# Optimization experiments

Hardware: AMD Instinct MI355X
Metric: run time of the kernel (lower is better)

## Reference

```python
import jax, jax.numpy as jnp
import numpy as np

EMB = 1024
HEADS = 16
HEADSIZE = EMB // HEADS
LN_EPS = 1e-5


def layernorm(x, w, b):
    # normalize over last dim (headsize)
    mu = jnp.mean(x, axis=-1, keepdims=True)
    var = jnp.var(x, axis=-1, keepdims=True)
    return (x - mu) * jax.lax.rsqrt(var + LN_EPS) * w + b


def setup_inputs() -> dict:
    key = jax.random.key(0)
    ks = jax.random.split(key, 8)
    B, S, C = 2, 2048, 2048
    x = jax.random.normal(ks[0], (B, S, EMB), dtype=jnp.float32)
    context = jax.random.normal(ks[1], (B, C, EMB), dtype=jnp.float32)
    mask = jnp.ones((B, S), dtype=jnp.float32)
    contextMask = jnp.ones((B, C), dtype=jnp.float32)
    s = 0.02
    Wq = jax.random.normal(ks[2], (EMB, EMB), dtype=jnp.float32) * s
    Wk = jax.random.normal(ks[3], (EMB, EMB), dtype=jnp.float32) * s
    Wv = jax.random.normal(ks[4], (EMB, EMB), dtype=jnp.float32) * s
    Wu = jax.random.normal(ks[5], (EMB, EMB), dtype=jnp.float32) * s
    bu = jnp.zeros((EMB,), dtype=jnp.float32)
    qln_w = jnp.ones((HEADSIZE,), dtype=jnp.float32)
    qln_b = jnp.zeros((HEADSIZE,), dtype=jnp.float32)
    kln_w = jnp.ones((HEADSIZE,), dtype=jnp.float32)
    kln_b = jnp.zeros((HEADSIZE,), dtype=jnp.float32)
    return {"x": x, "context": context, "mask": mask, "contextMask": contextMask,
            "Wq": Wq, "Wk": Wk, "Wv": Wv, "Wu": Wu, "bu": bu,
            "qln_w": qln_w, "qln_b": qln_b, "kln_w": kln_w, "kln_b": kln_b}


def reference(x, context, mask, contextMask, Wq, Wk, Wv, Wu, bu, qln_w, qln_b, kln_w, kln_b):
    B, S, E = x.shape
    C = context.shape[1]
    T = S + C
    xc = jnp.concatenate([x, context], axis=1)            # [B, T, E]
    q = (x @ Wq).reshape(B, S, HEADS, HEADSIZE)
    k = (xc @ Wk).reshape(B, T, HEADS, HEADSIZE)
    v = (xc @ Wv).reshape(B, T, HEADS, HEADSIZE)
    q = layernorm(q, qln_w, qln_b)
    k = layernorm(k, kln_w, kln_b)
    scale = E ** 0.25
    q = q / scale
    k = k / scale
    # [B, H, S, T] score matrix (explicitly materialized, as in the original)
    dot = jnp.einsum('bshd,bthd->bhst', q, k)
    mcat = jnp.concatenate([mask, contextMask], axis=1)   # [B, T]
    dotMask = mask[:, None, :, None] * mcat[:, None, None, :]  # [B,1,S,T]
    # hand-rolled masked softmax: softmax(dot*mask) * mask, renormalize
    p = jax.nn.softmax(dot * dotMask, axis=-1) * dotMask
    p = p / (jnp.sum(p, axis=-1, keepdims=True) + 1e-13)
    out = jnp.einsum('bhst,bthd->bshd', p, v).reshape(B, S, E)
    return out @ Wu + bu
```

## Files before the change

kernel.cpp:

```cpp
#include <hip/hip_runtime.h>
#include <hip/hip_bf16.h>
#include <cstdint>

#define B_SZ   2
#define S_LEN  2048
#define C_LEN  2048
#define T_LEN  4096
#define EMB_   1024
#define HEADS_ 16
#define D_     64

typedef __attribute__((ext_vector_type(8))) short bf16x8;
typedef __attribute__((ext_vector_type(4))) float f32x4;
typedef __attribute__((ext_vector_type(16))) float f32x16;
typedef __attribute__((ext_vector_type(2))) float f32x2;

__device__ __forceinline__ unsigned short f2bf(float f) {
    unsigned u = __builtin_bit_cast(unsigned, f);
    u += 0x7fffu + ((u >> 16) & 1u);
    return (unsigned short)(u >> 16);
}
__device__ __forceinline__ float bf2f(unsigned short h) {
    return __builtin_bit_cast(float, (unsigned)h << 16);
}

__global__ void build_xcb_k(const float* __restrict__ x, const float* __restrict__ ctx,
                            unsigned short* __restrict__ xcb) {
    int i = blockIdx.x * blockDim.x + threadIdx.x;
    size_t e8 = (size_t)i * 8;
    int b = (int)(e8 / ((size_t)T_LEN * EMB_));
    size_t rem = e8 % ((size_t)T_LEN * EMB_);
    int t = (int)(rem / EMB_);
    int c = (int)(rem % EMB_);
    const float* src = (t < S_LEN)
        ? &x[((size_t)b * S_LEN + t) * EMB_ + c]
        : &ctx[((size_t)b * C_LEN + (t - S_LEN)) * EMB_ + c];
    float4 v0 = ((const float4*)src)[0];
    float4 v1 = ((const float4*)src)[1];
    uint4 o;
    o.x = (unsigned)f2bf(v0.x) | ((unsigned)f2bf(v0.y) << 16);
    o.y = (unsigned)f2bf(v0.z) | ((unsigned)f2bf(v0.w) << 16);
    o.z = (unsigned)f2bf(v1.x) | ((unsigned)f2bf(v1.y) << 16);
    o.w = (unsigned)f2bf(v1.z) | ((unsigned)f2bf(v1.w) << 16);
    *(uint4*)&xcb[e8] = o;
}

__global__ void mcat_k(const float* __restrict__ mask, const float* __restrict__ cmask,
                       float* __restrict__ Mcat) {
    int i = blockIdx.x * 256 + threadIdx.x;
    int b = i / T_LEN, t = i % T_LEN;
    Mcat[i] = (t < S_LEN) ? mask[(size_t)b * S_LEN + t]
                          : cmask[(size_t)b * C_LEN + (t - S_LEN)];
}

__global__ void wtrans4_k(const float* __restrict__ W0, const float* __restrict__ W1,
                          const float* __restrict__ W2, const float* __restrict__ W3,
                          unsigned short* __restrict__ T0, unsigned short* __restrict__ T1,
                          unsigned short* __restrict__ T2, unsigned short* __restrict__ T3) {
    __shared__ __align__(16) unsigned short tile[64][72];
    int bx = blockIdx.x, by = blockIdx.y, bz = blockIdx.z;
    const float* W = (bz == 0) ? W0 : (bz == 1) ? W1 : (bz == 2) ? W2 : W3;
    unsigned short* WT = (bz == 0) ? T0 : (bz == 1) ? T1 : (bz == 2) ? T2 : T3;
    int tid = threadIdx.x;
#pragma unroll
    for (int r = 0; r < 4; ++r) {
        int idx = tid + r * 256;
        int row = idx >> 4, c4 = idx & 15;
        float4 v = ((const float4*)&W[((size_t)(by * 64 + row)) * EMB_ + bx * 64])[c4];
        tile[row][c4 * 4 + 0] = f2bf(v.x);
        tile[row][c4 * 4 + 1] = f2bf(v.y);
        tile[row][c4 * 4 + 2] = f2bf(v.z);
        tile[row][c4 * 4 + 3] = f2bf(v.w);
    }
    __syncthreads();
#pragma unroll
    for (int r = 0; r < 2; ++r) {
        int idx = tid + r * 256;
        int n = idx >> 3, k8 = idx & 7;
        uint4 o;
        unsigned q[4];
#pragma unroll
        for (int j = 0; j < 4; ++j)
            q[j] = (unsigned)tile[k8 * 8 + 2 * j][n] | ((unsigned)tile[k8 * 8 + 2 * j + 1][n] << 16);
        o.x = q[0]; o.y = q[1]; o.z = q[2]; o.w = q[3];
        *(uint4*)&WT[((size_t)(bx * 64 + n)) * EMB_ + by * 64 + k8 * 8] = o;
    }
}

__global__ __launch_bounds__(256) void gemm_qkv_k(
    const unsigned short* __restrict__ A,
    const unsigned short* __restrict__ Bt,
    unsigned short* __restrict__ Yk,
    unsigned short* __restrict__ Yv,
    unsigned short* __restrict__ Yq) {
    constexpr int KTOT = 1024, NTOT = 1024;
    int nt = blockIdx.x, mt = blockIdx.y;
    if (nt >= 16 && (mt & 31) >= 16) return;
    __shared__ __align__(16) unsigned short As[128 * 32];
    __shared__ __align__(16) unsigned short Bs[128 * 32];
    int in_row0 = mt * 128;
    unsigned short* Cout;
    int col0, out_row0;
    if (nt < 8)       { Cout = Yk; col0 = nt * 128;        out_row0 = mt * 128; }
    else if (nt < 16) { Cout = Yv; col0 = (nt - 8) * 128;  out_row0 = mt * 128; }
    else              { Cout = Yq; col0 = (nt - 16) * 128;
                        out_row0 = (mt >> 5) * 2048 + (mt & 31) * 128; }
    int tid = threadIdx.x, w = tid >> 6, l = tid & 63, l15 = l & 15, lg = l >> 4;
    int wr = (w >> 1) * 64, wc = (w & 1) * 64;

    f32x4 zero4 = {0.f, 0.f, 0.f, 0.f};
    f32x4 acc[4][4];
#pragma unroll
    for (int i = 0; i < 4; ++i)
#pragma unroll
        for (int j = 0; j < 4; ++j) acc[i][j] = zero4;

    for (int k0 = 0; k0 < KTOT; k0 += 32) {
#pragma unroll
        for (int j = 0; j < 2; ++j) {
            int o = tid * 16 + j * 4096;
            int row = o >> 6;
            int ke = (o & 63) >> 1;
            __builtin_amdgcn_global_load_lds(
                (const __attribute__((address_space(1))) void*)&A[(size_t)(in_row0 + row) * KTOT + k0 + ke],
                (__attribute__((address_space(3))) void*)&As[o >> 1], 16, 0, 0);
            __builtin_amdgcn_global_load_lds(
                (const __attribute__((address_space(1))) void*)&Bt[(size_t)(nt * 128 + row) * KTOT + k0 + ke],
                (__attribute__((address_space(3))) void*)&Bs[o >> 1], 16, 0, 0);
        }
        __syncthreads();
        bf16x8 af[4], bf[4];
#pragma unroll
        for (int fr = 0; fr < 4; ++fr)
            af[fr] = *(const bf16x8*)&As[(wr + fr * 16 + l15) * 32 + lg * 8];
#pragma unroll
        for (int fc = 0; fc < 4; ++fc)
            bf[fc] = *(const bf16x8*)&Bs[(wc + fc * 16 + l15) * 32 + lg * 8];
#pragma unroll
        for (int fr = 0; fr < 4; ++fr)
#pragma unroll
            for (int fc = 0; fc < 4; ++fc)
                acc[fr][fc] = __builtin_amdgcn_mfma_f32_16x16x32_bf16(af[fr], bf[fc], acc[fr][fc], 0, 0, 0);
        __syncthreads();
    }
#pragma unroll
    for (int fr = 0; fr < 4; ++fr) {
#pragma unroll
        for (int fc = 0; fc < 4; ++fc) {
            int row = out_row0 + wr + fr * 16 + lg * 4;
            int col = col0 + wc + fc * 16 + l15;
#pragma unroll
            for (int i = 0; i < 4; ++i)
                Cout[(size_t)(row + i) * NTOT + col] = f2bf(acc[fr][fc][i]);
        }
    }
}

template <bool F32OUT>
__global__ __launch_bounds__(256) void gemm_bt_k(
    const unsigned short* __restrict__ A,
    const unsigned short* __restrict__ Bt,
    void* __restrict__ Cout,
    const float* __restrict__ bias,
    int mtiles_per_chunk, int chunk_stride) {
    constexpr int KTOT = 1024, NTOT = 1024;
    __shared__ __align__(16) unsigned short As[128 * 32];
    __shared__ __align__(16) unsigned short Bs[128 * 32];
    int nt = blockIdx.x, mt = blockIdx.y;
    int in_row0 = (mt / mtiles_per_chunk) * chunk_stride + (mt % mtiles_per_chunk) * 128;
    int out_row0 = mt * 128;
    int tid = threadIdx.x, w = tid >> 6, l = tid & 63, l15 = l & 15, lg = l >> 4;
    int wr = (w >> 1) * 64, wc = (w & 1) * 64;

    f32x4 zero4 = {0.f, 0.f, 0.f, 0.f};
    f32x4 acc[4][4];
#pragma unroll
    for (int i = 0; i < 4; ++i)
#pragma unroll
        for (int j = 0; j < 4; ++j) acc[i][j] = zero4;

    for (int k0 = 0; k0 < KTOT; k0 += 32) {
#pragma unroll
        for (int j = 0; j < 2; ++j) {
            int o = tid * 16 + j * 4096;
            int row = o >> 6;
            int ke = (o & 63) >> 1;
            __builtin_amdgcn_global_load_lds(
                (const __attribute__((address_space(1))) void*)&A[(size_t)(in_row0 + row) * KTOT + k0 + ke],
                (__attribute__((address_space(3))) void*)&As[o >> 1], 16, 0, 0);
            __builtin_amdgcn_global_load_lds(
                (const __attribute__((address_space(1))) void*)&Bt[(size_t)(nt * 128 + row) * KTOT + k0 + ke],
                (__attribute__((address_space(3))) void*)&Bs[o >> 1], 16, 0, 0);
        }
        __syncthreads();
        bf16x8 af[4], bf[4];
#pragma unroll
        for (int fr = 0; fr < 4; ++fr)
            af[fr] = *(const bf16x8*)&As[(wr + fr * 16 + l15) * 32 + lg * 8];
#pragma unroll
        for (int fc = 0; fc < 4; ++fc)
            bf[fc] = *(const bf16x8*)&Bs[(wc + fc * 16 + l15) * 32 + lg * 8];
#pragma unroll
        for (int fr = 0; fr < 4; ++fr)
#pragma unroll
            for (int fc = 0; fc < 4; ++fc)
                acc[fr][fc] = __builtin_amdgcn_mfma_f32_16x16x32_bf16(af[fr], bf[fc], acc[fr][fc], 0, 0, 0);
        __syncthreads();
    }
#pragma unroll
    for (int fr = 0; fr < 4; ++fr) {
#pragma unroll
        for (int fc = 0; fc < 4; ++fc) {
            int row = out_row0 + wr + fr * 16 + lg * 4;
            int col = nt * 128 + wc + fc * 16 + l15;
#pragma unroll
            for (int i = 0; i < 4; ++i) {
                float v = acc[fr][fc][i];
                if (F32OUT) {
                    ((float*)Cout)[(size_t)(row + i) * NTOT + col] = v + bias[col];
                } else {
                    ((unsigned short*)Cout)[(size_t)(row + i) * NTOT + col] = f2bf(v);
                }
            }
        }
    }
}

__global__ void ln_head_k(const unsigned short* __restrict__ Y,
                          unsigned short* __restrict__ Out,
                          const float* __restrict__ lw, const float* __restrict__ lb,
                          const float* __restrict__ Mcat,
                          int rows_per_b, float scale) {
    int gw = blockIdx.x * 4 + (threadIdx.x >> 6);
    int lane = threadIdx.x & 63;
    int h = gw % HEADS_;
    int row = gw / HEADS_;
    int b = row / rows_per_b, r = row % rows_per_b;
    float v = bf2f(Y[(size_t)row * EMB_ + h * 64 + lane]);
    float s = v, s2 = v * v;
#pragma unroll
    for (int m = 1; m <= 32; m <<= 1) {
        s += __shfl_xor(s, m);
        s2 += __shfl_xor(s2, m);
    }
    float mu = s * (1.f / 64.f);
    float var = s2 * (1.f / 64.f) - mu * mu;
    float o = (v - mu) * rsqrtf(var + 1e-5f) * lw[lane] + lb[lane];
    float mq = Mcat[(size_t)b * T_LEN + r];
    Out[(((size_t)b * HEADS_ + h) * rows_per_b + r) * 64 + lane] = f2bf(o * scale * mq);
}

__global__ void ln_head_pack_k(const unsigned short* __restrict__ Y,
                               unsigned short* __restrict__ KF,
                               const float* __restrict__ lw, const float* __restrict__ lb,
                               const float* __restrict__ Mcat,
                               float scale) {
    int gw = blockIdx.x * 4 + (threadIdx.x >> 6);
    int lane = threadIdx.x & 63;
    int h = gw % HEADS_;
    int row = gw / HEADS_;
    int b = row / T_LEN, r = row % T_LEN;
    float v = bf2f(Y[(size_t)row * EMB_ + h * 64 + lane]);
    float s = v, s2 = v * v;
#pragma unroll
    for (int m = 1; m <= 32; m <<= 1) {
        s += __shfl_xor(s, m);
        s2 += __shfl_xor(s2, m);
    }
    float mu = s * (1.f / 64.f);
    float var = s2 * (1.f / 64.f) - mu * mu;
    float o = (v - mu) * rsqrtf(var + 1e-5f) * lw[lane] + lb[lane];
    float mt = Mcat[(size_t)b * T_LEN + r];
    int bh = b * HEADS_ + h;
    int kt = r >> 5, l31 = r & 31;
    int sf = lane >> 4, hi = (lane >> 3) & 1, j = lane & 7;
    size_t flat = ((((size_t)bh * 128 + kt) * 4 + sf) * 64 + hi * 32 + l31) * 8 + j;
    KF[flat] = f2bf(o * scale * mt);
}

__global__ void vpack_k(const unsigned short* __restrict__ Yv, unsigned short* __restrict__ VF,
                        const float* __restrict__ Mcat) {
    __shared__ __align__(16) unsigned short tile[64][72];
    __shared__ float msk[64];
    int t0 = blockIdx.x * 64;
    int bh = blockIdx.y;
    int b = bh >> 4, h = bh & 15;
    int tid = threadIdx.x;
    if (tid < 64) msk[tid] = Mcat[(size_t)b * T_LEN + t0 + tid];
#pragma unroll
    for (int rr = 0; rr < 2; ++rr) {
        int idx = tid + rr * 256;
        int row = idx >> 3, c8 = idx & 7;
        *(uint4*)&tile[row][c8 * 8] =
            *(const uint4*)&Yv[((size_t)b * T_LEN + t0 + row) * EMB_ + h * 64 + c8 * 8];
    }
    __syncthreads();
    int f = tid >> 6, l = tid & 63;
    int d = (f >> 1) * 32 + (l & 31);
    int tb = (f & 1) * 16 + 4 * (l >> 5);
#pragma unroll
    for (int ktl = 0; ktl < 2; ++ktl) {
        unsigned short e[8];
#pragma unroll
        for (int j = 0; j < 8; ++j) {
            int tt = ktl * 32 + tb + (j >> 2) * 8 + (j & 3);
            e[j] = f2bf(bf2f(tile[tt][d]) * msk[tt]);
        }
        uint4 o;
        o.x = (unsigned)e[0] | ((unsigned)e[1] << 16);
        o.y = (unsigned)e[2] | ((unsigned)e[3] << 16);
        o.z = (unsigned)e[4] | ((unsigned)e[5] << 16);
        o.w = (unsigned)e[6] | ((unsigned)e[7] << 16);
        size_t kt = (size_t)blockIdx.x * 2 + ktl;
        *(uint4*)&VF[((((size_t)bh * 128 + kt) * 4 + f) * 64 + l) * 8] = o;
    }
}

#define SOFTMAX(SA, LS, PB0, PB1) do {                                            \
    f32x2 e2[8];                                                                  \
    _Pragma("unroll") for (int i_ = 0; i_ < 8; ++i_) {                            \
        e2[i_][0] = __builtin_amdgcn_exp2f(SA[2 * i_]);                           \
        e2[i_][1] = __builtin_amdgcn_exp2f(SA[2 * i_ + 1]);                       \
    }                                                                             \
    {                                                                             \
        float rsA_ = 0.f, rsB_ = 0.f;                                             \
        _Pragma("unroll") for (int i_ = 0; i_ < 8; ++i_) {                        \
            rsA_ = fmaf(e2[i_][0], mt_[2 * i_], rsA_);                            \
            rsB_ = fmaf(e2[i_][1], mt_[2 * i_ + 1], rsB_);                        \
        }                                                                         \
        float rs_ = rsA_ + rsB_;                                                  \
        rs_ += __shfl_xor(rs_, 32);                                               \
        (LS) += rs_;                                                              \
    }                                                                             \
    unsigned pk_[8];                                                              \
    _Pragma("unroll") for (int d_ = 0; d_ < 8; ++d_)                              \
        asm("v_cvt_pk_bf16_f32 %0, %1, %2" : "=v"(pk_[d_])                        \
            : "v"(e2[d_][0]), "v"(e2[d_][1]));                                    \
    { uint4 u0_; u0_.x=pk_[0]; u0_.y=pk_[1]; u0_.z=pk_[2]; u0_.w=pk_[3];          \
      uint4 u1_; u1_.x=pk_[4]; u1_.y=pk_[5]; u1_.z=pk_[6]; u1_.w=pk_[7];          \
      (PB0) = __builtin_bit_cast(bf16x8, u0_);                                    \
      (PB1) = __builtin_bit_cast(bf16x8, u1_); }                                  \
} while (0)

#define LOADK(DST, KT) do {                                                       \
    const unsigned short* p_ = KFl + (size_t)(KT) * 2048;                         \
    DST[0] = *(const uint4*)(p_);                                                 \
    DST[1] = *(const uint4*)(p_ + 512);                                           \
    DST[2] = *(const uint4*)(p_ + 1024);                                          \
    DST[3] = *(const uint4*)(p_ + 1536);                                          \
} while (0)

#define LOADV(DST, KT) do {                                                       \
    const unsigned short* p_ = VFl + (size_t)(KT) * 2048;                         \
    DST[0] = *(const uint4*)(p_);                                                 \
    DST[1] = *(const uint4*)(p_ + 512);                                           \
    DST[2] = *(const uint4*)(p_ + 1024);                                          \
    DST[3] = *(const uint4*)(p_ + 1536);                                          \
} while (0)

__global__ __launch_bounds__(256) void attn32_k(
    const unsigned short* __restrict__ Q,
    const unsigned short* __restrict__ KF,
    const unsigned short* __restrict__ VF,
    const float* __restrict__ Mcat,
    unsigned short* __restrict__ O) {
    __shared__ float Olds[4][32][64];
    __shared__ float Llds[4][64];

    int bid = blockIdx.x;
    int xcd = bid & 7, slot = bid >> 3;
    int bh = xcd * 4 + (slot >> 5);
    int qblk = slot & 31;
    int b = bh >> 4, h = bh & 15;
    int tid = threadIdx.x;
    int w = tid >> 6;
    int lane = tid & 63;
    int l31 = lane & 31;
    int hi = lane >> 5;
    int q0 = qblk * 64;

    const unsigned short* KFl = KF + (size_t)bh * 262144 + lane * 8;
    const unsigned short* VFl = VF + (size_t)bh * 262144 + lane * 8;
    const float* Mb = Mcat + (size_t)b * T_LEN;

    bf16x8 qf0[4], qf1[4];
    {
        const unsigned short* Qp0 = Q + ((size_t)bh * S_LEN + q0 + l31) * 64 + hi * 8;
        const unsigned short* Qp1 = Qp0 + (size_t)32 * 64;
#pragma unroll
        for (int s = 0; s < 4; ++s) {
            qf0[s] = *(const bf16x8*)(Qp0 + s * 16);
            qf1[s] = *(const bf16x8*)(Qp1 + s * 16);
        }
    }

    f32x16 Z16;
#pragma unroll
    for (int i = 0; i < 16; ++i) Z16[i] = 0.f;
    f32x16 acc00 = Z16, acc01 = Z16, acc10 = Z16, acc11 = Z16;
    float lS0 = 0.f, lS1 = 0.f;

    auto TILE = [&](const uint4* kf, const uint4* vv, int kt) {
        const float* mbase = Mb + kt * 32 + 4 * hi;
        float4 mf0 = *(const float4*)(mbase);
        float4 mf1 = *(const float4*)(mbase + 8);
        float4 mf2 = *(const float4*)(mbase + 16);
        float4 mf3 = *(const float4*)(mbase + 24);
        f32x16 sa0 = Z16, sa1 = Z16;
#pragma unroll
        for (int s = 0; s < 4; ++s) {
            bf16x8 kfr = __builtin_bit_cast(bf16x8, kf[s]);
            sa0 = __builtin_amdgcn_mfma_f32_32x32x16_bf16(kfr, qf0[s], sa0, 0, 0, 0);
            sa1 = __builtin_amdgcn_mfma_f32_32x32x16_bf16(kfr, qf1[s], sa1, 0, 0, 0);
        }
        float mt_[16];
        mt_[0] = mf0.x; mt_[1] = mf0.y; mt_[2]  = mf0.z; mt_[3]  = mf0.w;
        mt_[4] = mf1.x; mt_[5] = mf1.y; mt_[6]  = mf1.z; mt_[7]  = mf1.w;
        mt_[8] = mf2.x; mt_[9] = mf2.y; mt_[10] = mf2.z; mt_[11] = mf2.w;
        mt_[12] = mf3.x; mt_[13] = mf3.y; mt_[14] = mf3.z; mt_[15] = mf3.w;
        bf16x8 p00, p01, p10, p11;
        SOFTMAX(sa0, lS0, p00, p01);
        SOFTMAX(sa1, lS1, p10, p11);
        bf16x8 vf;
        vf = __builtin_bit_cast(bf16x8, vv[0]);
        acc00 = __builtin_amdgcn_mfma_f32_32x32x16_bf16(vf, p00, acc00, 0, 0, 0);
        acc01 = __builtin_amdgcn_mfma_f32_32x32x16_bf16(vf, p10, acc01, 0, 0, 0);
        vf = __builtin_bit_cast(bf16x8, vv[1]);
        acc00 = __builtin_amdgcn_mfma_f32_32x32x16_bf16(vf, p01, acc00, 0, 0, 0);
        acc01 = __builtin_amdgcn_mfma_f32_32x32x16_bf16(vf, p11, acc01, 0, 0, 0);
        vf = __builtin_bit_cast(bf16x8, vv[2]);
        acc10 = __builtin_amdgcn_mfma_f32_32x32x16_bf16(vf, p00, acc10, 0, 0, 0);
        acc11 = __builtin_amdgcn_mfma_f32_32x32x16_bf16(vf, p10, acc11, 0, 0, 0);
        vf = __builtin_bit_cast(bf16x8, vv[3]);
        acc10 = __builtin_amdgcn_mfma_f32_32x32x16_bf16(vf, p01, acc10, 0, 0, 0);
        acc11 = __builtin_amdgcn_mfma_f32_32x32x16_bf16(vf, p11, acc11, 0, 0, 0);
    };

    uint4 ka[4], kb[4], va[4], vb[4];
    LOADK(ka, w); LOADV(va, w);
    for (int it = 0; it < 32; it += 2) {
        int kt0 = w + it * 4;
        LOADK(kb, kt0 + 4); LOADV(vb, kt0 + 4);
        TILE(ka, va, kt0);
        int nxt = (it + 2 < 32) ? kt0 + 8 : kt0;
        LOADK(ka, nxt); LOADV(va, nxt);
        TILE(kb, vb, kt0 + 4);
    }

    if (hi == 0) {
        Llds[w][l31] = lS0;
        Llds[w][32 + l31] = lS1;
    }
    int qm = tid & 63;
    float invL;

#pragma unroll
    for (int r = 0; r < 16; ++r) {
        int dl = (r & 3) + 8 * (r >> 2) + 4 * hi;
        Olds[w][dl][l31] = acc00[r];
        Olds[w][dl][32 + l31] = acc01[r];
    }
    __syncthreads();
    {
        float L = Llds[0][qm] + Llds[1][qm] + Llds[2][qm] + Llds[3][qm];
        invL = 1.f / (L + 1e-13f);
        float mqz = Mb[q0 + qm];
        invL = (mqz != 0.f) ? invL : 0.f;
    }
    {
        float v_[8];
#pragma unroll
        for (int dd = 0; dd < 8; ++dd) {
            int d = w * 8 + dd;
            v_[dd] = (Olds[0][d][qm] + Olds[1][d][qm] +
                      Olds[2][d][qm] + Olds[3][d][qm]) * invL;
        }
        unsigned po_[4];
#pragma unroll
        for (int d2 = 0; d2 < 4; ++d2)
            asm("v_cvt_pk_bf16_f32 %0, %1, %2" : "=v"(po_[d2]) : "v"(v_[2*d2]), "v"(v_[2*d2+1]));
        uint4 st; st.x = po_[0]; st.y = po_[1]; st.z = po_[2]; st.w = po_[3];
        *(uint4*)&O[((size_t)b * S_LEN + q0 + qm) * EMB_ + h * 64 + w * 8] = st;
    }
    __syncthreads();
#pragma unroll
    for (int r = 0; r < 16; ++r) {
        int dl = (r & 3) + 8 * (r >> 2) + 4 * hi;
        Olds[w][dl][l31] = acc10[r];
        Olds[w][dl][32 + l31] = acc11[r];
    }
    __syncthreads();
    {
        float v_[8];
#pragma unroll
        for (int dd = 0; dd < 8; ++dd) {
            int d = w * 8 + dd;
            v_[dd] = (Olds[0][d][qm] + Olds[1][d][qm] +
                      Olds[2][d][qm] + Olds[3][d][qm]) * invL;
        }
        unsigned po_[4];
#pragma unroll
        for (int d2 = 0; d2 < 4; ++d2)
            asm("v_cvt_pk_bf16_f32 %0, %1, %2" : "=v"(po_[d2]) : "v"(v_[2*d2]), "v"(v_[2*d2+1]));
        uint4 st; st.x = po_[0]; st.y = po_[1]; st.z = po_[2]; st.w = po_[3];
        *(uint4*)&O[((size_t)b * S_LEN + q0 + qm) * EMB_ + h * 64 + 32 + w * 8] = st;
    }
}

extern "C" void kernel_launch(void* const* d_in, const int* in_sizes, int n_in,
                              void* d_out, int out_size, void* d_ws, size_t ws_size,
                              hipStream_t stream) {
    const float* x     = (const float*)d_in[0];
    const float* ctx   = (const float*)d_in[1];
    const float* mask  = (const float*)d_in[2];
    const float* cmask = (const float*)d_in[3];
    const float* Wq    = (const float*)d_in[4];
    const float* Wk    = (const float*)d_in[5];
    const float* Wv    = (const float*)d_in[6];
    const float* Wu    = (const float*)d_in[7];
    const float* bu    = (const float*)d_in[8];
    const float* qlnw  = (const float*)d_in[9];
    const float* qlnb  = (const float*)d_in[10];
    const float* klnw  = (const float*)d_in[11];
    const float* klnb  = (const float*)d_in[12];

    unsigned short* ws = (unsigned short*)d_ws;
    unsigned short* xcb = ws + 0;
    unsigned short* WkT = ws + 8388608;
    unsigned short* WvT = ws + 9437184;
    unsigned short* WqT = ws + 10485760;
    unsigned short* Qb  = ws + 0;
    unsigned short* KFb = ws + 4194304;
    unsigned short* WuT = ws + 12582912;
    unsigned short* Yq  = ws + 13631488;
    unsigned short* Ob  = Yq;
    unsigned short* Yk  = ws + 17825792;
    unsigned short* VFb = Yk;
    unsigned short* Yv  = ws + 26214400;
    float* Mcat         = (float*)(ws + 34603008);

    const float scale = 0.17677669529663687f;
    const float qscale = 0.17677669529663687f * 1.4426950408889634f;

    build_xcb_k<<<4096, 256, 0, stream>>>(x, ctx, xcb);
    mcat_k<<<32, 256, 0, stream>>>(mask, cmask, Mcat);
    wtrans4_k<<<dim3(16, 16, 4), 256, 0, stream>>>(Wk, Wv, Wq, Wu, WkT, WvT, WqT, WuT);

    gemm_qkv_k<<<dim3(24, 64), 256, 0, stream>>>(xcb, WkT, Yk, Yv, Yq);

    ln_head_k<<<16384, 256, 0, stream>>>(Yq, Qb, qlnw, qlnb, Mcat, S_LEN, qscale);
    ln_head_pack_k<<<32768, 256, 0, stream>>>(Yk, KFb, klnw, klnb, Mcat, scale);
    vpack_k<<<dim3(64, 32), 256, 0, stream>>>(Yv, VFb, Mcat);

    attn32_k<<<1024, 256, 0, stream>>>(Qb, KFb, VFb, Mcat, Ob);

    gemm_bt_k<true><<<dim3(8, 32), 256, 0, stream>>>(Ob, WuT, d_out, bu, 32, 4096);
}
```

Measured before the change: 271.9 us.

## Share K/V tiles across waves via LDS double buffering in attention kernel

```diff
diff --git a/kernel.cpp b/kernel.cpp
--- a/kernel.cpp
+++ b/kernel.cpp
@@ -342,168 +342,121 @@
       (PB1) = __builtin_bit_cast(bf16x8, u1_); }                                  \
 } while (0)
 
-#define LOADK(DST, KT) do {                                                       \
-    const unsigned short* p_ = KFl + (size_t)(KT) * 2048;                         \
-    DST[0] = *(const uint4*)(p_);                                                 \
-    DST[1] = *(const uint4*)(p_ + 512);                                           \
-    DST[2] = *(const uint4*)(p_ + 1024);                                          \
-    DST[3] = *(const uint4*)(p_ + 1536);                                          \
-} while (0)
-
-#define LOADV(DST, KT) do {                                                       \
-    const unsigned short* p_ = VFl + (size_t)(KT) * 2048;                         \
-    DST[0] = *(const uint4*)(p_);                                                 \
-    DST[1] = *(const uint4*)(p_ + 512);                                           \
-    DST[2] = *(const uint4*)(p_ + 1024);                                          \
-    DST[3] = *(const uint4*)(p_ + 1536);                                          \
-} while (0)
-
 __global__ __launch_bounds__(256) void attn32_k(
     const unsigned short* __restrict__ Q,
     const unsigned short* __restrict__ KF,
     const unsigned short* __restrict__ VF,
     const float* __restrict__ Mcat,
     unsigned short* __restrict__ O) {
-    __shared__ float Olds[4][32][64];
-    __shared__ float Llds[4][64];
+    __shared__ __align__(16) unsigned short Ks[2][2048];
+    __shared__ __align__(16) unsigned short Vs[2][2048];
+    __shared__ float OldsF[4][64][32];
+    __shared__ float Llds[4][32];
 
     int bid = blockIdx.x;
     int xcd = bid & 7, slot = bid >> 3;
-    int bh = xcd * 4 + (slot >> 5);
-    int qblk = slot & 31;
+    int bh = xcd * 4 + (slot >> 4);
+    int qblk = slot & 15;
     int b = bh >> 4, h = bh & 15;
     int tid = threadIdx.x;
     int w = tid >> 6;
     int lane = tid & 63;
     int l31 = lane & 31;
     int hi = lane >> 5;
-    int q0 = qblk * 64;
-
-    const unsigned short* KFl = KF + (size_t)bh * 262144 + lane * 8;
-    const unsigned short* VFl = VF + (size_t)bh * 262144 + lane * 8;
+    int q0 = qblk * 128;
+    int qw = q0 + w * 32;
+
+    const unsigned short* KFb_ = KF + (size_t)bh * 262144;
+    const unsigned short* VFb_ = VF + (size_t)bh * 262144;
     const float* Mb = Mcat + (size_t)b * T_LEN;
 
-    bf16x8 qf0[4], qf1[4];
+    bf16x8 qf[4];
     {
-        const unsigned short* Qp0 = Q + ((size_t)bh * S_LEN + q0 + l31) * 64 + hi * 8;
-        const unsigned short* Qp1 = Qp0 + (size_t)32 * 64;
-#pragma unroll
-        for (int s = 0; s < 4; ++s) {
-            qf0[s] = *(const bf16x8*)(Qp0 + s * 16);
-            qf1[s] = *(const bf16x8*)(Qp1 + s * 16);
-        }
+        const unsigned short* Qp = Q + ((size_t)bh * S_LEN + qw + l31) * 64 + hi * 8;
+#pragma unroll
+        for (int s = 0; s < 4; ++s) qf[s] = *(const bf16x8*)(Qp + s * 16);
     }
 
     f32x16 Z16;
 #pragma unroll
     for (int i = 0; i < 16; ++i) Z16[i] = 0.f;
-    f32x16 acc00 = Z16, acc01 = Z16, acc10 = Z16, acc11 = Z16;
-    float lS0 = 0.f, lS1 = 0.f;
-
-    auto TILE = [&](const uint4* kf, const uint4* vv, int kt) {
+    f32x16 acc0 = Z16, acc1 = Z16;
+    float lS = 0.f;
+
+#define STAGE(BUF, KT) do {                                                        \
+    __builtin_amdgcn_global_load_lds(                                              \
+        (const __attribute__((address_space(1))) void*)(KFb_ + (size_t)(KT) * 2048 + tid * 8), \
+        (__attribute__((address_space(3))) void*)&Ks[BUF][tid * 8], 16, 0, 0);     \
+    __builtin_amdgcn_global_load_lds(                                              \
+        (const __attribute__((address_space(1))) void*)(VFb_ + (size_t)(KT) * 2048 + tid * 8), \
+        (__attribute__((address_space(3))) void*)&Vs[BUF][tid * 8], 16, 0, 0);     \
+} while (0)
+
+    STAGE(0, 0);
+    __syncthreads();
+
+    for (int kt = 0; kt < 128; ++kt) {
+        int cur = kt & 1;
+        if (kt + 1 < 128) STAGE(cur ^ 1, kt + 1);
         const float* mbase = Mb + kt * 32 + 4 * hi;
         float4 mf0 = *(const float4*)(mbase);
         float4 mf1 = *(const float4*)(mbase + 8);
         float4 mf2 = *(const float4*)(mbase + 16);
         float4 mf3 = *(const float4*)(mbase + 24);
-        f32x16 sa0 = Z16, sa1 = Z16;
+        bf16x8 kfr[4], vfr[4];
 #pragma unroll
         for (int s = 0; s < 4; ++s) {
-            bf16x8 kfr = __builtin_bit_cast(bf16x8, kf[s]);
-            sa0 = __builtin_amdgcn_mfma_f32_32x32x16_bf16(kfr, qf0[s], sa0, 0, 0, 0);
-            sa1 = __builtin_amdgcn_mfma_f32_32x32x16_bf16(kfr, qf1[s], sa1, 0, 0, 0);
-        }
+            kfr[s] = *(const bf16x8*)&Ks[cur][s * 512 + lane * 8];
+            vfr[s] = *(const bf16x8*)&Vs[cur][s * 512 + lane * 8];
+        }
+        f32x16 sa = Z16;
+#pragma unroll
+        for (int s = 0; s < 4; ++s)
+            sa = __builtin_amdgcn_mfma_f32_32x32x16_bf16(kfr[s], qf[s], sa, 0, 0, 0);
         float mt_[16];
         mt_[0] = mf0.x; mt_[1] = mf0.y; mt_[2]  = mf0.z; mt_[3]  = mf0.w;
         mt_[4] = mf1.x; mt_[5] = mf1.y; mt_[6]  = mf1.z; mt_[7]  = mf1.w;
         mt_[8] = mf2.x; mt_[9] = mf2.y; mt_[10] = mf2.z; mt_[11] = mf2.w;
         mt_[12] = mf3.x; mt_[13] = mf3.y; mt_[14] = mf3.z; mt_[15] = mf3.w;
-        bf16x8 p00, p01, p10, p11;
-        SOFTMAX(sa0, lS0, p00, p01);
-        SOFTMAX(sa1, lS1, p10, p11);
-        bf16x8 vf;
-        vf = __builtin_bit_cast(bf16x8, vv[0]);
-        acc00 = __builtin_amdgcn_mfma_f32_32x32x16_bf16(vf, p00, acc00, 0, 0, 0);
-        acc01 = __builtin_amdgcn_mfma_f32_32x32x16_bf16(vf, p10, acc01, 0, 0, 0);
-        vf = __builtin_bit_cast(bf16x8, vv[1]);
-        acc00 = __builtin_amdgcn_mfma_f32_32x32x16_bf16(vf, p01, acc00, 0, 0, 0);
-        acc01 = __builtin_amdgcn_mfma_f32_32x32x16_bf16(vf, p11, acc01, 0, 0, 0);
-        vf = __builtin_bit_cast(bf16x8, vv[2]);
-        acc10 = __builtin_amdgcn_mfma_f32_32x32x16_bf16(vf, p00, acc10, 0, 0, 0);
-        acc11 = __builtin_amdgcn_mfma_f32_32x32x16_bf16(vf, p10, acc11, 0, 0, 0);
-        vf = __builtin_bit_cast(bf16x8, vv[3]);
-        acc10 = __builtin_amdgcn_mfma_f32_32x32x16_bf16(vf, p01, acc10, 0, 0, 0);
-        acc11 = __builtin_amdgcn_mfma_f32_32x32x16_bf16(vf, p11, acc11, 0, 0, 0);
-    };
-
-    uint4 ka[4], kb[4], va[4], vb[4];
-    LOADK(ka, w); LOADV(va, w);
-    for (int it = 0; it < 32; it += 2) {
-        int kt0 = w + it * 4;
-        LOADK(kb, kt0 + 4); LOADV(vb, kt0 + 4);
-        TILE(ka, va, kt0);
-        int nxt = (it + 2 < 32) ? kt0 + 8 : kt0;
-        LOADK(ka, nxt); LOADV(va, nxt);
-        TILE(kb, vb, kt0 + 4);
-    }
-
-    if (hi == 0) {
-        Llds[w][l31] = lS0;
-        Llds[w][32 + l31] = lS1;
-    }
-    int qm = tid & 63;
-    float invL;
+        bf16x8 p0, p1;
+        SOFTMAX(sa, lS, p0, p1);
+        acc0 = __builtin_amdgcn_mfma_f32_32x32x16_bf16(vfr[0], p0, acc0, 0, 0, 0);
+        acc0 = __builtin_amdgcn_mfma_f32_32x32x16_bf16(vfr[1], p1, acc0, 0, 0, 0);
+        acc1 = __builtin_amdgcn_mfma_f32_32x32x16_bf16(vfr[2], p0, acc1, 0, 0, 0);
+        acc1 = __builtin_amdgcn_mfma_f32_32x32x16_bf16(vfr[3], p1, acc1, 0, 0, 0);
+        __syncthreads();
+    }
+#undef STAGE
 
 #pragma unroll
     for (int r = 0; r < 16; ++r) {
         int dl = (r & 3) + 8 * (r >> 2) + 4 * hi;
-        Olds[w][dl][l31] = acc00[r];
-        Olds[w][dl][32 + l31] = acc01[r];
-    }
+        OldsF[w][dl][l31] = acc0[r];
+        OldsF[w][dl + 32][l31] = acc1[r];
+    }
+    if (hi == 0) Llds[w][l31] = lS;
     __syncthreads();
     {
-        float L = Llds[0][qm] + Llds[1][qm] + Llds[2][qm] + Llds[3][qm];
-        invL = 1.f / (L + 1e-13f);
-        float mqz = Mb[q0 + qm];
+        int rr = lane >> 1, hf = lane & 1;
+        float L = Llds[w][rr];
+        float invL = 1.f / (L + 1e-13f);
+        float mqz = Mb[q0 + w * 32 + rr];
         invL = (mqz != 0.f) ? invL : 0.f;
-    }
-    {
-        float v_[8];
-#pragma unroll
-        for (int dd = 0; dd < 8; ++dd) {
-            int d = w * 8 + dd;
-            v_[dd] = (Olds[0][d][qm] + Olds[1][d][qm] +
-                      Olds[2][d][qm] + Olds[3][d][qm]) * invL;
-        }
-        unsigned po_[4];
-#pragma unroll
-        for (int d2 = 0; d2 < 4; ++d2)
+        float v_[32];
+#pragma unroll
+        for (int dd = 0; dd < 32; ++dd)
+            v_[dd] = OldsF[w][hf * 32 + dd][rr] * invL;
+        unsigned po_[16];
+#pragma unroll
+        for (int d2 = 0; d2 < 16; ++d2)
             asm("v_cvt_pk_bf16_f32 %0, %1, %2" : "=v"(po_[d2]) : "v"(v_[2*d2]), "v"(v_[2*d2+1]));
-        uint4 st; st.x = po_[0]; st.y = po_[1]; st.z = po_[2]; st.w = po_[3];
-        *(uint4*)&O[((size_t)b * S_LEN + q0 + qm) * EMB_ + h * 64 + w * 8] = st;
-    }
-    __syncthreads();
-#pragma unroll
-    for (int r = 0; r < 16; ++r) {
-        int dl = (r & 3) + 8 * (r >> 2) + 4 * hi;
-        Olds[w][dl][l31] = acc10[r];
-        Olds[w][dl][32 + l31] = acc11[r];
-    }
-    __syncthreads();
-    {
-        float v_[8];
-#pragma unroll
-        for (int dd = 0; dd < 8; ++dd) {
-            int d = w * 8 + dd;
-            v_[dd] = (Olds[0][d][qm] + Olds[1][d][qm] +
-                      Olds[2][d][qm] + Olds[3][d][qm]) * invL;
-        }
-        unsigned po_[4];
-#pragma unroll
-        for (int d2 = 0; d2 < 4; ++d2)
-            asm("v_cvt_pk_bf16_f32 %0, %1, %2" : "=v"(po_[d2]) : "v"(v_[2*d2]), "v"(v_[2*d2+1]));
-        uint4 st; st.x = po_[0]; st.y = po_[1]; st.z = po_[2]; st.w = po_[3];
-        *(uint4*)&O[((size_t)b * S_LEN + q0 + qm) * EMB_ + h * 64 + 32 + w * 8] = st;
+        unsigned short* Orow = &O[((size_t)b * S_LEN + qw + rr) * EMB_ + h * 64 + hf * 32];
+#pragma unroll
+        for (int i = 0; i < 4; ++i) {
+            uint4 st;
+            st.x = po_[4*i]; st.y = po_[4*i+1]; st.z = po_[4*i+2]; st.w = po_[4*i+3];
+            *(uint4*)(Orow + i * 8) = st;
+        }
     }
 }
 
@@ -552,7 +505,7 @@
     ln_head_pack_k<<<32768, 256, 0, stream>>>(Yk, KFb, klnw, klnb, Mcat, scale);
     vpack_k<<<dim3(64, 32), 256, 0, stream>>>(Yv, VFb, Mcat);
 
-    attn32_k<<<1024, 256, 0, stream>>>(Qb, KFb, VFb, Mcat, Ob);
+    attn32_k<<<512, 256, 0, stream>>>(Qb, KFb, VFb, Mcat, Ob);
 
     gemm_bt_k<true><<<dim3(8, 32), 256, 0, stream>>>(Ob, WuT, d_out, bu, 32, 4096);
 }
```

New measurement: 265.9 us. -2.2%, faster.
